# Optimization experiments

Measured on AMD Instinct MI355X. Metric: run time of the kernel, lower is better.

The kernel has to match this reference:

```python
import jax, jax.numpy as jnp
import numpy as np

_SAMPLING_EPS = 1e-5


def setup_inputs() -> dict:
    key = jax.random.key(0)
    k0, k1, k2, k3, k4, k5, k6 = jax.random.split(key, 7)
    T, D, V, B = 8192, 4096, 32000, 64  # total tokens, hidden, vocab, num seqs
    hidden_states = jax.random.normal(k0, (T, D), jnp.float32)
    embedding = jax.random.normal(k1, (V, D), jnp.float32) * 0.02
    last_token_indices = jnp.sort(jax.random.randint(k2, (B,), 0, T)).astype(jnp.int64)
    temperatures = jax.random.uniform(k3, (B,), jnp.float32)  # in (0,1)
    top_ps = jax.random.uniform(k4, (B,), jnp.float32)
    top_ks = jax.random.randint(k5, (B,), 1, 1000).astype(jnp.int64)
    u = jax.random.uniform(k6, (B,), jnp.float32)  # inverse-CDF sample draw
    return {
        "hidden_states": hidden_states,
        "embedding": embedding,
        "temperatures": temperatures,
        "top_ps": top_ps,
        "u": u,
        "last_token_indices": last_token_indices,
        "top_ks": top_ks,
    }


def reference(hidden_states, embedding, temperatures, top_ps, u,
              last_token_indices, top_ks):
    V = embedding.shape[0]
    # _prune_hidden_states: keep last token of each sequence -> [B, D]
    h = hidden_states[last_token_indices]
    # _get_logits: [B, V]
    logits = jnp.einsum("bd,vd->bv", h, embedding)
    # temperature scaling (temps < eps treated as 1.0, greedy handled upstream)
    temps = jnp.where(temperatures < _SAMPLING_EPS, 1.0, temperatures)
    logits = logits / temps[:, None]
    probs = jax.nn.softmax(logits.astype(jnp.float32), axis=-1)

    # sort descending once; do top-k and top-p filtering in sorted space
    order = jnp.argsort(-probs, axis=-1)                 # [B, V]
    sorted_p = jnp.take_along_axis(probs, order, axis=-1)
    k = jnp.clip(top_ks, 1, V).astype(jnp.int32)
    kth = jnp.take_along_axis(sorted_p, (k - 1)[:, None], axis=-1)  # [B,1]
    f = jnp.where(sorted_p >= kth, sorted_p, 0.0)        # top-k filter
    cum = jnp.cumsum(f, axis=-1)
    # keep index i iff cumsum up to i-1 <= top_p (first element always kept)
    keep_p = ((cum - f) <= top_ps[:, None]) | (top_ps[:, None] >= 1.0 - _SAMPLING_EPS)
    f = jnp.where(keep_p, f, 0.0)
    total = jnp.sum(f, axis=-1, keepdims=True)
    # fallback to unfiltered probs if everything got zeroed
    f = jnp.where(total > 0, f, sorted_p)
    total = jnp.sum(f, axis=-1, keepdims=True)

    # multinomial via inverse CDF in sorted space
    cdf = jnp.cumsum(f, axis=-1)
    j = jnp.sum(cdf < u[:, None] * total, axis=-1)
    j = jnp.clip(j, 0, V - 1)
    tokens = jnp.take_along_axis(order, j[:, None], axis=-1).reshape(-1)

    # filtered normalized probs back in token order (for inspection/grads)
    inv = jnp.argsort(order, axis=-1)
    probs_final = jnp.take_along_axis(f / total, inv, axis=-1)
    return tokens, probs_final
```

## Files before the change

kernel.cpp:

```cpp
#include <hip/hip_runtime.h>
#include <stdint.h>

#define D_DIM 4096
#define V_DIM 32000
#define B_SEQ 64
#define MAXC 2048
#define SPLITK 4
#define KCH 1024

typedef __attribute__((ext_vector_type(8))) short short8;
typedef __attribute__((ext_vector_type(4))) float f32x4;

#define H1_OFF     0u
#define H2_OFF     131072u
#define H3_OFF     262144u
#define LOGITS_OFF 393216u
#define PART_OFF   2441216u

#define GLD16(gsrc, ldst) \
    __builtin_amdgcn_global_load_lds((const __attribute__((address_space(1))) unsigned*)(gsrc), \
                                     (__attribute__((address_space(3))) unsigned*)(ldst), 16, 0, 0)

__device__ __forceinline__ unsigned f2key(float x) {
    unsigned u = __float_as_uint(x);
    return (u & 0x80000000u) ? ~u : (u | 0x80000000u);
}
__device__ __forceinline__ float key2f(unsigned k) {
    unsigned u = (k & 0x80000000u) ? (k & 0x7FFFFFFFu) : ~k;
    return __uint_as_float(u);
}
__device__ __forceinline__ void split3(float x, ushort& a, ushort& b, ushort& c) {
    unsigned u = __float_as_uint(x);
    a = (ushort)(u >> 16);
    float r1 = x - __uint_as_float(u & 0xFFFF0000u);
    unsigned u2 = __float_as_uint(r1);
    b = (ushort)(u2 >> 16);
    float r2 = r1 - __uint_as_float(u2 & 0xFFFF0000u);
    c = (ushort)(__float_as_uint(r2) >> 16);
}

__global__ void k_prep(const float* __restrict__ hs, const int* __restrict__ lti,
                       ushort* __restrict__ h1, ushort* __restrict__ h2,
                       ushort* __restrict__ h3) {
    int b = blockIdx.x;
    const float4* src = (const float4*)(hs + (size_t)lti[b] * D_DIM);
    ushort4* d1 = (ushort4*)(h1 + (size_t)b * D_DIM);
    ushort4* d2 = (ushort4*)(h2 + (size_t)b * D_DIM);
    ushort4* d3 = (ushort4*)(h3 + (size_t)b * D_DIM);
    for (int i = threadIdx.x; i < D_DIM / 4; i += blockDim.x) {
        float4 v = src[i];
        float x[4] = {v.x, v.y, v.z, v.w};
        ushort l1[4], l2[4], l3[4];
#pragma unroll
        for (int j = 0; j < 4; ++j) split3(x[j], l1[j], l2[j], l3[j]);
        d1[i] = make_ushort4(l1[0], l1[1], l1[2], l1[3]);
        d2[i] = make_ushort4(l2[0], l2[1], l2[2], l2[3]);
        d3[i] = make_ushort4(l3[0], l3[1], l3[2], l3[3]);
    }
}

__device__ __forceinline__ void splitB(const float4& x0, const float4& x1,
                                       short8& b1, short8& b2, short8& b3) {
    float xf[8] = {x0.x, x0.y, x0.z, x0.w, x1.x, x1.y, x1.z, x1.w};
#pragma unroll
    for (int j = 0; j < 8; ++j) {
        ushort u1, u2, u3;
        split3(xf[j], u1, u2, u3);
        b1[j] = (short)u1; b2[j] = (short)u2; b3[j] = (short)u3;
    }
}

__global__ __launch_bounds__(256, 2) void k_gemm(const ushort* __restrict__ h1,
                                                 const ushort* __restrict__ h2,
                                                 const ushort* __restrict__ h3,
                                                 const float* __restrict__ emb,
                                                 float* __restrict__ part) {
    __shared__ __align__(16) float  sB[2][4096];
    __shared__ __align__(16) ushort sA1[2][4096];
    __shared__ __align__(16) ushort sA2[2][4096];
    __shared__ __align__(16) ushort sA3[2][4096];
    const int tid = threadIdx.x;
    const int w = tid >> 6, lane = tid & 63, lrow = lane & 15, q = lane >> 4;
    const int kc = blockIdx.y;
    const int vbase = blockIdx.x * 64;
    const int vrow = vbase + w * 16 + lrow;
    const size_t kbase = (size_t)kc * KCH;

    f32x4 acc[4];
#pragma unroll
    for (int mf = 0; mf < 4; ++mf)
#pragma unroll
        for (int r = 0; r < 4; ++r) acc[mf][r] = 0.f;

    const float* srcB[4];
#pragma unroll
    for (int j = 0; j < 4; ++j) {
        int row = w * 4 + j * 16 + (lane >> 4);
        unsigned c16 = (((unsigned)(lane & 15)) << 4) ^ (((unsigned)(row & 7)) << 4);
        srcB[j] = emb + (size_t)(vbase + row) * D_DIM + kbase + (c16 >> 2);
    }
    const ushort* srcA1[2]; const ushort* srcA2[2]; const ushort* srcA3[2];
#pragma unroll
    for (int j = 0; j < 2; ++j) {
        int row = w * 8 + j * 32 + (lane >> 3);
        unsigned c16 = (((unsigned)(lane & 7)) << 4) ^ (((unsigned)(row & 7)) << 4);
        size_t off = (size_t)row * D_DIM + kbase + (c16 >> 1);
        srcA1[j] = h1 + off; srcA2[j] = h2 + off; srcA3[j] = h3 + off;
    }
    const unsigned brow = (unsigned)(w * 16 + lrow);
    const unsigned bswz = (brow & 7u) << 4;
    const unsigned ldst = (unsigned)(w * 1024);

#define STAGE(nb, kk) do { \
        GLD16(srcB[0] + (kk), (char*)&sB[nb][0]  + ldst + 0);     \
        GLD16(srcB[1] + (kk), (char*)&sB[nb][0]  + ldst + 4096);  \
        GLD16(srcB[2] + (kk), (char*)&sB[nb][0]  + ldst + 8192);  \
        GLD16(srcB[3] + (kk), (char*)&sB[nb][0]  + ldst + 12288); \
        GLD16(srcA1[0] + (kk), (char*)&sA1[nb][0] + ldst + 0);    \
        GLD16(srcA1[1] + (kk), (char*)&sA1[nb][0] + ldst + 4096); \
        GLD16(srcA2[0] + (kk), (char*)&sA2[nb][0] + ldst + 0);    \
        GLD16(srcA2[1] + (kk), (char*)&sA2[nb][0] + ldst + 4096); \
        GLD16(srcA3[0] + (kk), (char*)&sA3[nb][0] + ldst + 0);    \
        GLD16(srcA3[1] + (kk), (char*)&sA3[nb][0] + ldst + 4096); \
    } while (0)

    STAGE(0, 0);
    __syncthreads();

    for (int k0 = 0; k0 < KCH; k0 += 64) {
        const int cur = (k0 >> 6) & 1;
        if (k0 + 64 < KCH) STAGE(cur ^ 1, k0 + 64);
        const char* bb = (const char*)&sB[cur][0] + brow * 256u;
        const char* a1b = (const char*)&sA1[cur][0];
        const char* a2b = (const char*)&sA2[cur][0];
        const char* a3b = (const char*)&sA3[cur][0];
#pragma unroll
        for (int s = 0; s < 2; ++s) {
            unsigned binner = (unsigned)(s * 128 + q * 32);
            float4 bf0 = *(const float4*)(bb + (binner ^ bswz));
            float4 bf1 = *(const float4*)(bb + ((binner + 16u) ^ bswz));
            short8 vb1, vb2, vb3;
            splitB(bf0, bf1, vb1, vb2, vb3);
#pragma unroll
            for (int mf = 0; mf < 4; ++mf) {
                unsigned arow = (unsigned)(mf * 16 + lrow);
                unsigned abyte = arow * 128u
                               + (((unsigned)(s * 64 + q * 16)) ^ ((arow & 7u) << 4));
                short8 a1 = *(const short8*)(a1b + abyte);
                short8 a2 = *(const short8*)(a2b + abyte);
                short8 a3 = *(const short8*)(a3b + abyte);
                acc[mf] = __builtin_amdgcn_mfma_f32_16x16x32_bf16(a1, vb1, acc[mf], 0, 0, 0);
                acc[mf] = __builtin_amdgcn_mfma_f32_16x16x32_bf16(a1, vb2, acc[mf], 0, 0, 0);
                acc[mf] = __builtin_amdgcn_mfma_f32_16x16x32_bf16(a2, vb1, acc[mf], 0, 0, 0);
                acc[mf] = __builtin_amdgcn_mfma_f32_16x16x32_bf16(a2, vb2, acc[mf], 0, 0, 0);
                acc[mf] = __builtin_amdgcn_mfma_f32_16x16x32_bf16(a1, vb3, acc[mf], 0, 0, 0);
                acc[mf] = __builtin_amdgcn_mfma_f32_16x16x32_bf16(a3, vb1, acc[mf], 0, 0, 0);
            }
        }
        __syncthreads();
    }
#undef STAGE
    float* pout = part + (size_t)kc * (B_SEQ * V_DIM);
#pragma unroll
    for (int mf = 0; mf < 4; ++mf)
#pragma unroll
        for (int r = 0; r < 4; ++r) {
            int m = mf * 16 + q * 4 + r;
            pout[(size_t)m * V_DIM + vrow] = acc[mf][r];
        }
}

__device__ __forceinline__ float4 f4add(float4 a, float4 b) {
    return make_float4(a.x + b.x, a.y + b.y, a.z + b.z, a.w + b.w);
}

__global__ void k_reduce(const float* __restrict__ part,
                         const float* __restrict__ temps,
                         float* __restrict__ logits,
                         float* __restrict__ out_probs) {
    const int b = blockIdx.y;
    float t = temps[b];
    if (t < 1e-5f) t = 1.0f;
    const float inv = 1.0f / t;
    const float4* p0 = (const float4*)(part + 0 * (size_t)(B_SEQ * V_DIM) + (size_t)b * V_DIM);
    const float4* p1 = (const float4*)(part + 1 * (size_t)(B_SEQ * V_DIM) + (size_t)b * V_DIM);
    const float4* p2 = (const float4*)(part + 2 * (size_t)(B_SEQ * V_DIM) + (size_t)b * V_DIM);
    const float4* p3 = (const float4*)(part + 3 * (size_t)(B_SEQ * V_DIM) + (size_t)b * V_DIM);
    float4* lo = (float4*)(logits + (size_t)b * V_DIM);
    float4* po = (float4*)(out_probs + (size_t)b * V_DIM);
    const float4 z4 = make_float4(0.f, 0.f, 0.f, 0.f);
    for (int i = blockIdx.x * 256 + threadIdx.x; i < V_DIM / 4; i += 2048) {
        float4 s = f4add(f4add(f4add(p0[i], p1[i]), p2[i]), p3[i]);
        lo[i] = make_float4(s.x * inv, s.y * inv, s.z * inv, s.w * inv);
        po[i] = z4;
    }
}

__global__ __launch_bounds__(512) void k_sample(const float* __restrict__ logits,
                                                const int* __restrict__ tks,
                                                const float* __restrict__ tps,
                                                const float* __restrict__ uu,
                                                float* __restrict__ out_tok,
                                                float* __restrict__ out_probs) {
    const int b = blockIdx.x, t = threadIdx.x;
    const float* lr = logits + (size_t)b * V_DIM;
    __shared__ unsigned hist[2048];
    __shared__ unsigned redu[512];
    __shared__ float redf[512];
    __shared__ unsigned long long cand[MAXC];
    __shared__ float sp[MAXC];
    __shared__ unsigned s_sel1, s_ab1, s_thr, s_nc, s_ab2, s_kthkey;
    __shared__ float s_m, s_Z, s_tot;
    __shared__ int s_cnt, s_L, s_tok, s_nk;

    int k = tks[b];
    if (k < 1) k = 1;
    if (k > V_DIM) k = V_DIM;

    for (int i = t; i < 2048; i += 512) hist[i] = 0u;
    __syncthreads();
    unsigned km = 0u;
    for (int v = t; v < V_DIM; v += 512) {
        unsigned key = f2key(lr[v]);
        km = max(km, key);
        atomicAdd(&hist[key >> 21], 1u);
    }
    redu[t] = km;
    __syncthreads();
    for (int s = 256; s > 0; s >>= 1) {
        if (t < s) redu[t] = max(redu[t], redu[t + s]);
        __syncthreads();
    }
    if (t == 0) s_m = key2f(redu[0]);
    __syncthreads();
    float m = s_m;
    redu[t] = hist[4 * t] + hist[4 * t + 1] + hist[4 * t + 2] + hist[4 * t + 3];
    __syncthreads();
    if (t == 0) {
        unsigned acc = 0; int g = 0; bool found = false;
        for (int g0 = 511; g0 >= 0 && !found; g0 -= 8) {
            unsigned v[8];
#pragma unroll
            for (int j = 0; j < 8; ++j) v[j] = redu[g0 - j];
#pragma unroll
            for (int j = 0; j < 8; ++j) {
                if (acc + v[j] >= (unsigned)k) { g = g0 - j; found = true; break; }
                acc += v[j];
            }
        }
        int sel = 4 * g;
        for (int bk = 4 * g + 3; bk >= 4 * g; --bk) {
            unsigned h = hist[bk];
            if (acc + h >= (unsigned)k) { sel = bk; break; }
            acc += h;
        }
        s_sel1 = (unsigned)sel; s_ab1 = acc;
    }
    __syncthreads();
    unsigned sel1 = s_sel1, ab1 = s_ab1;

    for (int i = t; i < 2048; i += 512) hist[i] = 0u;
    __syncthreads();
    float es = 0.f;
    for (int v = t; v < V_DIM; v += 512) {
        float f = lr[v];
        es += expf(f - m);
        unsigned key = f2key(f);
        if ((key >> 21) == sel1) atomicAdd(&hist[(key >> 10) & 2047u], 1u);
    }
    redf[t] = es;
    __syncthreads();
    for (int s = 256; s > 0; s >>= 1) {
        if (t < s) redf[t] += redf[t + s];
        __syncthreads();
    }
    if (t == 0) s_Z = redf[0];
    __syncthreads();
    redu[t] = hist[4 * t] + hist[4 * t + 1] + hist[4 * t + 2] + hist[4 * t + 3];
    __syncthreads();
    if (t == 0) {
        unsigned kk = (unsigned)k - ab1;
        unsigned acc = 0; int g = 0; bool found = false;
        for (int g0 = 511; g0 >= 0 && !found; g0 -= 8) {
            unsigned v[8];
#pragma unroll
            for (int j = 0; j < 8; ++j) v[j] = redu[g0 - j];
#pragma unroll
            for (int j = 0; j < 8; ++j) {
                if (acc + v[j] >= kk) { g = g0 - j; found = true; break; }
                acc += v[j];
            }
        }
        int sel = 4 * g;
        for (int bk = 4 * g + 3; bk >= 4 * g; --bk) {
            unsigned h = hist[bk];
            if (acc + h >= kk) { sel = bk; break; }
            acc += h;
        }
        s_ab2 = ab1 + acc;
        s_thr = (sel1 << 21) | ((unsigned)sel << 10);
        s_nc = ab1 + acc + hist[sel];
    }
    __syncthreads();
    unsigned thr = s_thr;

    if (s_nc > (unsigned)MAXC) {
        for (int i = t; i < 1024; i += 512) hist[i] = 0u;
        __syncthreads();
        for (int v = t; v < V_DIM; v += 512) {
            unsigned key = f2key(lr[v]);
            if ((key & 0xFFFFFC00u) == thr) atomicAdd(&hist[key & 1023u], 1u);
        }
        __syncthreads();
        if (t == 0) {
            unsigned kk = (unsigned)k - s_ab2;
            unsigned acc = 0; int sel = 0;
            for (int bk = 1023; bk >= 0; --bk) {
                unsigned h = hist[bk];
                if (acc + h >= kk) { sel = bk; break; }
                acc += h;
            }
            s_thr = thr | (unsigned)sel;
        }
        __syncthreads();
        thr = s_thr;
    }

    if (t == 0) s_cnt = 0;
    for (int i = t; i < MAXC; i += 512) cand[i] = 0xFFFFFFFFFFFFFFFFULL;
    __syncthreads();
    for (int v = t; v < V_DIM; v += 512) {
        unsigned key = f2key(lr[v]);
        if (key >= thr) {
            int p = atomicAdd(&s_cnt, 1);
            if (p < MAXC) cand[p] = (((unsigned long long)(~key)) << 32) | (unsigned)v;
        }
    }
    __syncthreads();
    int n = s_cnt; if (n > MAXC) n = MAXC;
    const int np2 = (n <= 1) ? 1 : (1 << (32 - __clz(n - 1)));

    for (unsigned size = 2; size <= (unsigned)np2; size <<= 1)
        for (unsigned stride = size >> 1; stride > 0; stride >>= 1) {
            for (unsigned i = t; i < (unsigned)np2; i += 512) {
                unsigned j = i ^ stride;
                if (j > i) {
                    unsigned long long a = cand[i], c = cand[j];
                    bool up = ((i & size) == 0);
                    if (up ? (a > c) : (a < c)) { cand[i] = c; cand[j] = a; }
                }
            }
            __syncthreads();
        }
    float Z = s_Z;
    for (int i = t; i < n; i += 512) {
        unsigned key = ~(unsigned)(cand[i] >> 32);
        sp[i] = expf(key2f(key) - m) / Z;
    }
    for (int i = n + t; i < MAXC; i += 512) sp[i] = 0.f;
    if (t == 0) s_kthkey = ~(unsigned)(cand[k - 1] >> 32);
    __syncthreads();

    unsigned kthkey = s_kthkey;
    int cnt = 0;
    for (int i = t; i < n; i += 512)
        if ((~(unsigned)(cand[i] >> 32)) >= kthkey) cnt++;
    redu[t] = (unsigned)cnt;
    __syncthreads();
    for (int s = 256; s > 0; s >>= 1) {
        if (t < s) redu[t] += redu[t + s];
        __syncthreads();
    }
    if (t == 0) s_nk = (int)redu[0];
    __syncthreads();

    if (t == 0) {
        float top_p = tps[b];
        bool keepall = (top_p >= 1.0f - 1e-5f);
        int limit = min(n, s_nk);
        float c = 0.f; int L = limit; bool done = false;
        for (int i0 = 0; i0 < limit && !done; i0 += 8) {
            float v[8];
#pragma unroll
            for (int j = 0; j < 8; ++j) v[j] = sp[i0 + j];
#pragma unroll
            for (int j = 0; j < 8; ++j) {
                int i = i0 + j;
                if (i >= limit) { done = true; break; }
                float cum = c + v[j];
                if (!keepall && !((cum - v[j]) <= top_p)) { L = i; done = true; break; }
                c = cum;
            }
        }
        float total = c;
        float target = uu[b] * total;
        float c2 = 0.f; int jj = L - 1; done = false;
        for (int i0 = 0; i0 < L && !done; i0 += 8) {
            float v[8];
#pragma unroll
            for (int j = 0; j < 8; ++j) v[j] = sp[i0 + j];
#pragma unroll
            for (int j = 0; j < 8; ++j) {
                int i = i0 + j;
                if (i >= L) { done = true; break; }
                c2 += v[j];
                if (!(c2 < target)) { jj = i; done = true; break; }
            }
        }
        s_tok = (int)(cand[jj] & 0xFFFFFFFFULL);
        s_L = L; s_tot = total;
        out_tok[b] = (float)s_tok;
    }
    __syncthreads();
    int L = s_L; float total = s_tot;
    for (int i = t; i < L; i += 512) {
        unsigned v = (unsigned)(cand[i] & 0xFFFFFFFFULL);
        out_probs[(size_t)b * V_DIM + v] = sp[i] / total;
    }
}

extern "C" void kernel_launch(void* const* d_in, const int* in_sizes, int n_in,
                              void* d_out, int out_size, void* d_ws, size_t ws_size,
                              hipStream_t stream) {
    const float* hs    = (const float*)d_in[0];
    const float* emb   = (const float*)d_in[1];
    const float* temps = (const float*)d_in[2];
    const float* tps   = (const float*)d_in[3];
    const float* uu    = (const float*)d_in[4];
    const int*   lti   = (const int*)d_in[5];
    const int*   tks   = (const int*)d_in[6];

    float* ws = (float*)d_ws;
    ushort* h1 = (ushort*)(ws + H1_OFF);
    ushort* h2 = (ushort*)(ws + H2_OFF);
    ushort* h3 = (ushort*)(ws + H3_OFF);
    float* logits = ws + LOGITS_OFF;
    float* part   = ws + PART_OFF;

    float* out_tok   = (float*)d_out;
    float* out_probs = (float*)d_out + B_SEQ;

    k_prep<<<B_SEQ, 256, 0, stream>>>(hs, lti, h1, h2, h3);
    k_gemm<<<dim3(V_DIM / 64, SPLITK), 256, 0, stream>>>(h1, h2, h3, emb, part);
    k_reduce<<<dim3(8, B_SEQ), 256, 0, stream>>>(part, temps, logits, out_probs);
    k_sample<<<B_SEQ, 512, 0, stream>>>(logits, tks, tps, uu, out_tok, out_probs);
}
```

Measured before the change: 312.7 us.

## Overlap next-tile global-to-LDS loads with MFMA via partial vmcnt waits

Reworks the double-buffered K loop of the split-K GEMM. Each iteration now issues the next tile's global_load_lds, waits only until the previous tile's loads have landed (vmcnt(10)) instead of a full __syncthreads drain, and pins ordering with sched_barrier and s_barrier. The last tile is peeled out of the loop. MFMA sections are wrapped in s_setprio to raise wave priority during compute. The aim is to stop every barrier from draining the prefetch so loads and matrix math overlap. The risk is subtle correctness issues if the outstanding-load count assumption is wrong.

After: 327.1 us. 1.05x slower.

```diff
diff --git a/kernel.cpp b/kernel.cpp
--- a/kernel.cpp
+++ b/kernel.cpp
@@ -124,42 +124,56 @@
         GLD16(srcA3[1] + (kk), (char*)&sA3[nb][0] + ldst + 4096); \
     } while (0)
 
+#define COMPUTE_TILE(cur) do {                                                        \
+        _Pragma("unroll")                                                             \
+        for (int s = 0; s < 2; ++s) {                                                 \
+            unsigned binner = (unsigned)(s * 128 + q * 32);                           \
+            const char* bb = (const char*)&sB[cur][0] + brow * 256u;                  \
+            float4 bf0 = *(const float4*)(bb + (binner ^ bswz));                      \
+            float4 bf1 = *(const float4*)(bb + ((binner + 16u) ^ bswz));              \
+            short8 vb1, vb2, vb3;                                                     \
+            splitB(bf0, bf1, vb1, vb2, vb3);                                          \
+            __builtin_amdgcn_s_setprio(1);                                            \
+            _Pragma("unroll")                                                         \
+            for (int mf = 0; mf < 4; ++mf) {                                          \
+                unsigned arow = (unsigned)(mf * 16 + lrow);                           \
+                unsigned abyte = arow * 128u                                          \
+                               + (((unsigned)(s * 64 + q * 16)) ^ ((arow & 7u) << 4));\
+                short8 a1 = *(const short8*)((const char*)&sA1[cur][0] + abyte);      \
+                short8 a2 = *(const short8*)((const char*)&sA2[cur][0] + abyte);      \
+                short8 a3 = *(const short8*)((const char*)&sA3[cur][0] + abyte);      \
+                acc[mf] = __builtin_amdgcn_mfma_f32_16x16x32_bf16(a1, vb1, acc[mf], 0, 0, 0); \
+                acc[mf] = __builtin_amdgcn_mfma_f32_16x16x32_bf16(a1, vb2, acc[mf], 0, 0, 0); \
+                acc[mf] = __builtin_amdgcn_mfma_f32_16x16x32_bf16(a2, vb1, acc[mf], 0, 0, 0); \
+                acc[mf] = __builtin_amdgcn_mfma_f32_16x16x32_bf16(a2, vb2, acc[mf], 0, 0, 0); \
+                acc[mf] = __builtin_amdgcn_mfma_f32_16x16x32_bf16(a1, vb3, acc[mf], 0, 0, 0); \
+                acc[mf] = __builtin_amdgcn_mfma_f32_16x16x32_bf16(a3, vb1, acc[mf], 0, 0, 0); \
+            }                                                                         \
+            __builtin_amdgcn_s_setprio(0);                                            \
+        }                                                                             \
+    } while (0)
+
     STAGE(0, 0);
-    __syncthreads();
-
-    for (int k0 = 0; k0 < KCH; k0 += 64) {
+
+    for (int k0 = 0; k0 < KCH - 64; k0 += 64) {
         const int cur = (k0 >> 6) & 1;
-        if (k0 + 64 < KCH) STAGE(cur ^ 1, k0 + 64);
-        const char* bb = (const char*)&sB[cur][0] + brow * 256u;
-        const char* a1b = (const char*)&sA1[cur][0];
-        const char* a2b = (const char*)&sA2[cur][0];
-        const char* a3b = (const char*)&sA3[cur][0];
-#pragma unroll
-        for (int s = 0; s < 2; ++s) {
-            unsigned binner = (unsigned)(s * 128 + q * 32);
-            float4 bf0 = *(const float4*)(bb + (binner ^ bswz));
-            float4 bf1 = *(const float4*)(bb + ((binner + 16u) ^ bswz));
-            short8 vb1, vb2, vb3;
-            splitB(bf0, bf1, vb1, vb2, vb3);
-#pragma unroll
-            for (int mf = 0; mf < 4; ++mf) {
-                unsigned arow = (unsigned)(mf * 16 + lrow);
-                unsigned abyte = arow * 128u
-                               + (((unsigned)(s * 64 + q * 16)) ^ ((arow & 7u) << 4));
-                short8 a1 = *(const short8*)(a1b + abyte);
-                short8 a2 = *(const short8*)(a2b + abyte);
-                short8 a3 = *(const short8*)(a3b + abyte);
-                acc[mf] = __builtin_amdgcn_mfma_f32_16x16x32_bf16(a1, vb1, acc[mf], 0, 0, 0);
-                acc[mf] = __builtin_amdgcn_mfma_f32_16x16x32_bf16(a1, vb2, acc[mf], 0, 0, 0);
-                acc[mf] = __builtin_amdgcn_mfma_f32_16x16x32_bf16(a2, vb1, acc[mf], 0, 0, 0);
-                acc[mf] = __builtin_amdgcn_mfma_f32_16x16x32_bf16(a2, vb2, acc[mf], 0, 0, 0);
-                acc[mf] = __builtin_amdgcn_mfma_f32_16x16x32_bf16(a1, vb3, acc[mf], 0, 0, 0);
-                acc[mf] = __builtin_amdgcn_mfma_f32_16x16x32_bf16(a3, vb1, acc[mf], 0, 0, 0);
-            }
-        }
-        __syncthreads();
-    }
+        STAGE(cur ^ 1, k0 + 64);
+        asm volatile("s_waitcnt vmcnt(10)" ::: "memory");
+        __builtin_amdgcn_sched_barrier(0);
+        __builtin_amdgcn_s_barrier();
+        __builtin_amdgcn_sched_barrier(0);
+        COMPUTE_TILE(cur);
+        __builtin_amdgcn_sched_barrier(0);
+        __builtin_amdgcn_s_barrier();
+    }
+    asm volatile("s_waitcnt vmcnt(0)" ::: "memory");
+    __builtin_amdgcn_sched_barrier(0);
+    __builtin_amdgcn_s_barrier();
+    __builtin_amdgcn_sched_barrier(0);
+    COMPUTE_TILE(1);
 #undef STAGE
+#undef COMPUTE_TILE
+
     float* pout = part + (size_t)kc * (B_SEQ * V_DIM);
 #pragma unroll
     for (int mf = 0; mf < 4; ++mf)
```
